# Kernel optimization log

Measured on AMD Instinct MI355X. Metric: run time of the kernel, lower is better.

Reference implementation:

```python
import jax, jax.numpy as jnp
import numpy as np

EPS = 1e-4
B, C, H, W = 8, 192, 64, 64
HID, DE, N_CLS, CLS_F, E = 256, 64, 8192, 128, 131072
N_IMG = B * H * W


def geolin(x, w):
    # MP_GeoLinear forward: weight-normalized linear, recomputed each call.
    fan = w.shape[1]
    n = jnp.linalg.norm(w, axis=1, keepdims=True)           # per-output-row norm (fp32)
    wn = w / (EPS + n / np.sqrt(fan))                       # normalize() with alpha=1/sqrt(fan)
    return x @ (wn * (1.0 / np.sqrt(fan))).T                # gain/sqrt(fan_in)


def mp_silu(x):
    return jax.nn.silu(x) / 0.596


def mp_cat(a, b, t=0.5):
    Na, Nb = a.shape[1], b.shape[1]
    Cc = np.sqrt((Na + Nb) / ((1 - t) ** 2 + t ** 2))
    return jnp.concatenate([(Cc / np.sqrt(Na) * (1 - t)) * a,
                            (Cc / np.sqrt(Nb) * t) * b], axis=1)


def hetero_conv(x_src, x_dst, src, dst, ea, wl, wr, n_dst):
    # MP_HIPGnnConv: gather -> mp_cat with edge_attr -> mean aggregate -> lin_l,
    # mp_sum with lin_r(x_dst) -> L2 normalize (normalize=True).
    msg = mp_cat(x_src[src], ea)                            # [E, HID+DE]
    s = jax.ops.segment_sum(msg, dst, num_segments=n_dst)
    cnt = jax.ops.segment_sum(jnp.ones((msg.shape[0],), msg.dtype), dst, num_segments=n_dst)
    agg = s / jnp.maximum(cnt, 1.0)[:, None]                # scatter-mean (empty rows -> 0)
    out = (geolin(agg, wl) + geolin(x_dst, wr)) / np.sqrt(2.0)  # mp_sum(t=0.5)
    return out / jnp.maximum(jnp.linalg.norm(out, axis=-1, keepdims=True), 1e-12)


def forward(x, class_x, ea_c2i, ea_i2c,
            w_in_img, w_in_cls,
            wl_c2i_1, wr_c2i_1, wl_i2c_1, wr_i2c_1,
            wl_c2i_2, wr_c2i_2, wl_i2c_2, wr_i2c_2,
            w_out_img, w_out_cls,
            src_c2i, dst_c2i, src_i2c, dst_i2c):
    b, c, h, w = x.shape
    n_img = b * h * w
    n_cls = class_x.shape[0]
    # image pixels become 'image_node' features: [B,C,H,W] -> [B*H*W, C]
    h_img = geolin(jnp.transpose(x, (0, 2, 3, 1)).reshape(-1, c), w_in_img)
    h_cls = geolin(class_x, w_in_cls)
    layers = [(wl_c2i_1, wr_c2i_1, wl_i2c_1, wr_i2c_1),
              (wl_c2i_2, wr_c2i_2, wl_i2c_2, wr_i2c_2)]
    for wl_ci, wr_ci, wl_ic, wr_ic in layers:
        a_img, a_cls = mp_silu(h_img), mp_silu(h_cls)
        h_img = hetero_conv(a_cls, a_img, src_c2i, dst_c2i, ea_c2i, wl_ci, wr_ci, n_img)
        h_cls = hetero_conv(a_img, a_cls, src_i2c, dst_i2c, ea_i2c, wl_ic, wr_ic, n_cls)
    out_img = geolin(h_img, w_out_img).reshape(b, h, w, -1)
    out_img = jnp.transpose(out_img, (0, 3, 1, 2))          # extract_image_nodes
    out_cls = geolin(h_cls, w_out_cls)
    return out_img, out_cls


def setup_inputs() -> dict:
    key = jax.random.key(0)
    ks = jax.random.split(key, 24)
    d = {
        'x': jax.random.normal(ks[0], (B, C, H, W), jnp.float32),
        'class_x': jax.random.normal(ks[1], (N_CLS, CLS_F), jnp.float32),
        'ea_c2i': jax.random.normal(ks[2], (E, DE), jnp.float32),
        'ea_i2c': jax.random.normal(ks[3], (E, DE), jnp.float32),
        'w_in_img': jax.random.normal(ks[4], (HID, C), jnp.float32),
        'w_in_cls': jax.random.normal(ks[5], (HID, CLS_F), jnp.float32),
        'wl_c2i_1': jax.random.normal(ks[6], (HID, HID + DE), jnp.float32),
        'wr_c2i_1': jax.random.normal(ks[7], (HID, HID), jnp.float32),
        'wl_i2c_1': jax.random.normal(ks[8], (HID, HID + DE), jnp.float32),
        'wr_i2c_1': jax.random.normal(ks[9], (HID, HID), jnp.float32),
        'wl_c2i_2': jax.random.normal(ks[10], (HID, HID + DE), jnp.float32),
        'wr_c2i_2': jax.random.normal(ks[11], (HID, HID), jnp.float32),
        'wl_i2c_2': jax.random.normal(ks[12], (HID, HID + DE), jnp.float32),
        'wr_i2c_2': jax.random.normal(ks[13], (HID, HID), jnp.float32),
        'w_out_img': jax.random.normal(ks[14], (HID, HID), jnp.float32),
        'w_out_cls': jax.random.normal(ks[15], (HID, HID), jnp.float32),
        'src_c2i': jax.random.randint(ks[16], (E,), 0, N_CLS, jnp.int32),
        'dst_c2i': jax.random.randint(ks[17], (E,), 0, N_IMG, jnp.int32),
        'src_i2c': jax.random.randint(ks[18], (E,), 0, N_IMG, jnp.int32),
        'dst_i2c': jax.random.randint(ks[19], (E,), 0, N_CLS, jnp.int32),
    }
    return d


def reference(x, class_x, ea_c2i, ea_i2c,
              w_in_img, w_in_cls,
              wl_c2i_1, wr_c2i_1, wl_i2c_1, wr_i2c_1,
              wl_c2i_2, wr_c2i_2, wl_i2c_2, wr_i2c_2,
              w_out_img, w_out_cls,
              src_c2i, dst_c2i, src_i2c, dst_i2c):
    return forward(x, class_x, ea_c2i, ea_i2c,
                   w_in_img, w_in_cls,
                   wl_c2i_1, wr_c2i_1, wl_i2c_1, wr_i2c_1,
                   wl_c2i_2, wr_c2i_2, wl_i2c_2, wr_i2c_2,
                   w_out_img, w_out_cls,
                   src_c2i, dst_c2i, src_i2c, dst_i2c)
```

## Files before the change

### kernel.cpp

```cpp
#include <hip/hip_runtime.h>
#include <cmath>

constexpr int CIN  = 192;
constexpr int HW   = 4096;
constexpr int NIMG = 32768;
constexpr int NCLS = 8192;
constexpr int NE   = 131072;

#define EPSW 1e-4f
#define ALPHA 0.7905694150420949f
#define BETA  1.5811388300841898f
#define SILU_INV 1.6778523489932886f

using bf16x8 = __attribute__((ext_vector_type(8))) __bf16;
using f32x4  = __attribute__((ext_vector_type(4))) float;

__device__ __forceinline__ ushort f2bf(float f) {
  uint u = __float_as_uint(f);
  u = (u + 0x7FFFu + ((u >> 16) & 1u)) >> 16;
  return (ushort)u;
}
__device__ __forceinline__ float bf2f(ushort h) {
  return __uint_as_float(((uint)h) << 16);
}
__device__ __forceinline__ float bflo(uint u) { return __uint_as_float(u << 16); }
__device__ __forceinline__ float bfhi(uint u) { return __uint_as_float(u & 0xFFFF0000u); }
__device__ __forceinline__ uint bfpack(float lo, float hi) {
  return (uint)f2bf(lo) | ((uint)f2bf(hi) << 16);
}
__device__ __forceinline__ float wave_red_sum(float v) {
  #pragma unroll
  for (int off = 32; off > 0; off >>= 1) v += __shfl_xor(v, off, 64);
  return v;
}
__device__ __forceinline__ int wave_red_sumi(int v) {
  #pragma unroll
  for (int off = 32; off > 0; off >>= 1) v += __shfl_xor(v, off, 64);
  return v;
}

struct WNA {
  const float* w[12];
  ushort* o[12];
  int F[12];
  int os[12];
  int oo[12];
};
__global__ __launch_bounds__(256) void pre_k(WNA a,
                                             const int* __restrict__ d1,
                                             const int* __restrict__ d2,
                                             int* __restrict__ c1,
                                             int* __restrict__ c2,
                                             const float* __restrict__ x,
                                             ushort* __restrict__ Xin,
                                             const float* __restrict__ clsx,
                                             ushort* __restrict__ clsb) {
  __shared__ ushort T[192 * 65];
  const int bx = blockIdx.x, t = threadIdx.x;
  if (bx < 768) {
    const int wi = bx >> 6;
    const int row = ((bx & 63) << 2) + (t >> 6);
    const int lane = t & 63;
    const int F = a.F[wi];
    const float* wr = a.w[wi] + (size_t)row * F;
    float ss = 0.f;
    for (int f = lane; f < F; f += 64) { float v = wr[f]; ss += v * v; }
    ss = wave_red_sum(ss);
    const float scale = 1.0f / (EPSW * sqrtf((float)F) + sqrtf(ss));
    ushort* o = a.o[wi] + (size_t)row * a.os[wi] + a.oo[wi];
    for (int f = lane; f < F; f += 64) o[f] = f2bf(wr[f] * scale);
  } else if (bx < 1280) {
    const int e = (bx - 768) * 256 + t;
    atomicAdd(&c1[d1[e]], 1);
    atomicAdd(&c2[d2[e]], 1);
  } else if (bx < 1792) {
    const int b2 = bx - 1280;
    const int b = b2 >> 6, hw0 = (b2 & 63) * 64;
    const float* xb = x + (size_t)b * CIN * HW;
    for (int idx = t; idx < CIN * 64; idx += 256) {
      int c = idx >> 6, p = idx & 63;
      T[c * 65 + p] = f2bf(xb[(size_t)c * HW + hw0 + p]);
    }
    __syncthreads();
    ushort* ob = Xin + ((size_t)b * HW + hw0) * CIN;
    for (int idx = t; idx < CIN * 64; idx += 256) {
      int p = idx / CIN, c = idx - p * CIN;
      ob[(size_t)p * CIN + c] = T[c * 65 + p];
    }
  } else {
    const int b3 = bx - 1792;
    for (int i4 = b3 * 256 + t; i4 < (NCLS * 128) / 4; i4 += 128 * 256) {
      float4 v = *(const float4*)(clsx + (size_t)i4 * 4);
      ushort4 o = { f2bf(v.x), f2bf(v.y), f2bf(v.z), f2bf(v.w) };
      *(ushort4*)(clsb + (size_t)i4 * 4) = o;
    }
  }
}

__global__ __launch_bounds__(256) void scanA_k(const int* __restrict__ cnt,
                                               int* __restrict__ st_img,
                                               int* __restrict__ st_cls,
                                               int* __restrict__ bsum) {
  const int bid = blockIdx.x;
  const bool cls = bid >= 32;
  const int* c = cnt + (cls ? NIMG : 0);
  int* s = cls ? st_cls : st_img;
  const int base = (cls ? bid - 32 : bid) * 1024;
  const int t = threadIdx.x, lane = t & 63, wid = t >> 6;
  int4 v = *(const int4*)(c + base + t * 4);
  const int i0 = v.x, i1 = i0 + v.y, i2 = i1 + v.z, i3 = i2 + v.w;
  int x = i3;
  #pragma unroll
  for (int off = 1; off < 64; off <<= 1) {
    int y = __shfl_up(x, off, 64);
    if (lane >= off) x += y;
  }
  const int pre = x - i3;
  __shared__ int wt[4];
  if (lane == 63) wt[wid] = x;
  __syncthreads();
  int woff = 0;
  #pragma unroll
  for (int i = 0; i < 4; ++i) if (i < wid) woff += wt[i];
  const int b = woff + pre;
  int4 o = { b, b + i0, b + i1, b + i2 };
  *(int4*)(s + base + t * 4) = o;
  if (t == 255) bsum[bid] = woff + x;
}

__global__ __launch_bounds__(256) void scanC_k(const int* __restrict__ bsum,
                                               int* __restrict__ st_img,
                                               int* __restrict__ st_cls) {
  const int bid = blockIdx.x;
  const bool cls = bid >= 32;
  const int seg0 = cls ? 32 : 0;
  const int t = threadIdx.x;
  __shared__ int off_s;
  if (t < 64) {
    int v = (t < bid - seg0) ? bsum[seg0 + t] : 0;
    v = wave_red_sumi(v);
    if (t == 0) off_s = v;
  }
  __syncthreads();
  const int off = off_s;
  int* s = cls ? st_cls : st_img;
  const int base = (cls ? bid - 32 : bid) * 1024;
  int4 v = *(int4*)(s + base + t * 4);
  v.x += off; v.y += off; v.z += off; v.w += off;
  *(int4*)(s + base + t * 4) = v;
  if (bid == 0 && t == 0) { st_img[NIMG] = NE; st_cls[NCLS] = NE; }
}

__global__ void fill2_k(const int* __restrict__ dst1, const int* __restrict__ src1,
                        const int* __restrict__ st1, int* __restrict__ cur1,
                        int2* __restrict__ eix1,
                        const int* __restrict__ dst2, const int* __restrict__ src2,
                        const int* __restrict__ st2, int* __restrict__ cur2,
                        int2* __restrict__ eix2) {
  int e = blockIdx.x * 256 + threadIdx.x;
  int d = dst1[e];
  int p = atomicAdd(&cur1[d], 1);
  eix1[st1[d] + p] = make_int2(e, src1[e]);
  d = dst2[e];
  p = atomicAdd(&cur2[d], 1);
  eix2[st2[d] + p] = make_int2(e, src2[e]);
}

__global__ void silu2_k(const ushort* __restrict__ Hi, const ushort* __restrict__ Hc,
                        ushort* __restrict__ Ai, ushort* __restrict__ Ac) {
  const size_t nimg = (size_t)NIMG * 256;
  size_t i8 = ((size_t)blockIdx.x * 256 + threadIdx.x) * 8;
  const ushort* in; ushort* out; size_t idx;
  if (i8 < nimg) { in = Hi; out = Ai; idx = i8; }
  else           { in = Hc; out = Ac; idx = i8 - nimg; }
  uint4 v = *(const uint4*)(in + idx);
  uint r[4];
  uint uu[4] = { v.x, v.y, v.z, v.w };
  #pragma unroll
  for (int i = 0; i < 4; ++i) {
    float lo = bflo(uu[i]), hi = bfhi(uu[i]);
    lo = (lo / (1.0f + __expf(-lo))) * SILU_INV;
    hi = (hi / (1.0f + __expf(-hi))) * SILU_INV;
    r[i] = bfpack(lo, hi);
  }
  uint4 o = { r[0], r[1], r[2], r[3] };
  *(uint4*)(out + idx) = o;
}

__global__ __launch_bounds__(256) void rownorm2_k(ushort* __restrict__ Hi,
                                                  ushort* __restrict__ Hc) {
  const int row  = blockIdx.x * 4 + (threadIdx.x >> 6);
  const int lane = threadIdx.x & 63;
  ushort* H = (row < NIMG) ? Hi + (size_t)row * 256
                           : Hc + (size_t)(row - NIMG) * 256;
  uint2 v = *(uint2*)(H + lane * 4);
  float x0 = bflo(v.x), x1 = bfhi(v.x), x2 = bflo(v.y), x3 = bfhi(v.y);
  float ss = x0 * x0 + x1 * x1 + x2 * x2 + x3 * x3;
  ss = wave_red_sum(ss);
  const float sc = 1.0f / fmaxf(sqrtf(ss), 1e-12f);
  uint2 o = { bfpack(x0 * sc, x1 * sc), bfpack(x2 * sc, x3 * sc) };
  *(uint2*)(H + lane * 4) = o;
}

__global__ __launch_bounds__(256) void agg2_k(
    const ushort* __restrict__ Aimg, const ushort* __restrict__ Acls,
    const int2* __restrict__ eix_ci, const int2* __restrict__ eix_ic,
    const int* __restrict__ st_img, const int* __restrict__ st_cls,
    ushort* __restrict__ agg_img, ushort* __restrict__ agg_cls,
    const float* __restrict__ ea_ci, const float* __restrict__ ea_ic,
    ushort* __restrict__ eam_img, ushort* __restrict__ eam_cls, int do_eam) {
  const int row = blockIdx.x * 8 + (threadIdx.x >> 5);
  const int hl  = threadIdx.x & 31;
  const ushort* Hs; const int2* eix; const int* st; ushort* out;
  const float* EA; ushort* oute; int r;
  if (row < NIMG) { r = row;        Hs = Acls; eix = eix_ci; st = st_img;
                    out = agg_img + (size_t)r * 256; EA = ea_ci;
                    oute = eam_img + (size_t)r * 64; }
  else            { r = row - NIMG; Hs = Aimg; eix = eix_ic; st = st_cls;
                    out = agg_cls + (size_t)r * 256; EA = ea_ic;
                    oute = eam_cls + (size_t)r * 64; }
  const int s0 = st[r], s1 = st[r + 1];
  float a[8] = {};
  float ae0 = 0.f, ae1 = 0.f;
  for (int j = s0; j < s1; j += 4) {
    const int i1 = min(j + 1, s1 - 1), i2 = min(j + 2, s1 - 1), i3 = min(j + 3, s1 - 1);
    const int2 e0 = eix[j], e1 = eix[i1], e2 = eix[i2], e3 = eix[i3];
    const float w1 = (j + 1 < s1) ? 1.f : 0.f;
    const float w2 = (j + 2 < s1) ? 1.f : 0.f;
    const float w3 = (j + 3 < s1) ? 1.f : 0.f;
    uint4 h0 = *(const uint4*)(Hs + (size_t)e0.y * 256 + hl * 8);
    uint4 h1 = *(const uint4*)(Hs + (size_t)e1.y * 256 + hl * 8);
    uint4 h2 = *(const uint4*)(Hs + (size_t)e2.y * 256 + hl * 8);
    uint4 h3 = *(const uint4*)(Hs + (size_t)e3.y * 256 + hl * 8);
    const uint u0[4] = { h0.x, h0.y, h0.z, h0.w };
    const uint u1[4] = { h1.x, h1.y, h1.z, h1.w };
    const uint u2[4] = { h2.x, h2.y, h2.z, h2.w };
    const uint u3[4] = { h3.x, h3.y, h3.z, h3.w };
    #pragma unroll
    for (int i = 0; i < 4; ++i) {
      a[2 * i + 0] += bflo(u0[i]) + w1 * bflo(u1[i]) + w2 * bflo(u2[i]) + w3 * bflo(u3[i]);
      a[2 * i + 1] += bfhi(u0[i]) + w1 * bfhi(u1[i]) + w2 * bfhi(u2[i]) + w3 * bfhi(u3[i]);
    }
    if (do_eam) {
      float2 v0 = *(const float2*)(EA + (size_t)e0.x * 64 + hl * 2);
      float2 v1 = *(const float2*)(EA + (size_t)e1.x * 64 + hl * 2);
      float2 v2 = *(const float2*)(EA + (size_t)e2.x * 64 + hl * 2);
      float2 v3 = *(const float2*)(EA + (size_t)e3.x * 64 + hl * 2);
      ae0 += v0.x + w1 * v1.x + w2 * v2.x + w3 * v3.x;
      ae1 += v0.y + w1 * v1.y + w2 * v2.y + w3 * v3.y;
    }
  }
  const float inv = 1.0f / fmaxf((float)(s1 - s0), 1.0f);
  const float c = ALPHA * inv;
  uint4 o;
  o.x = bfpack(a[0] * c, a[1] * c);
  o.y = bfpack(a[2] * c, a[3] * c);
  o.z = bfpack(a[4] * c, a[5] * c);
  o.w = bfpack(a[6] * c, a[7] * c);
  *(uint4*)(out + hl * 8) = o;
  if (do_eam) {
    const float cb = BETA * inv;
    *(uint*)(oute + hl * 2) = bfpack(ae0 * cb, ae1 * cb);
  }
}

__device__ __forceinline__ int lds_swz(int row, int kbyte) {
  return ((row << 6) + kbyte) ^ ((row & 7) << 4);
}

struct GJ {
  const ushort* A; const ushort* AG; const ushort* EAM; const ushort* B;
  void* O;
  int K, a_mode, c_mode, nrt;
};

__device__ __forceinline__ void gemm_body(const GJ J, int bx, char* ldsb) {
  ushort* As = (ushort*)ldsb;
  ushort* Bs = (ushort*)(ldsb + 8192);
  const int t    = threadIdx.x;
  const int row0 = (bx % J.nrt) * 128;
  const int col0 = (bx / J.nrt) * 128;
  const int srow = t >> 1;
  const int skh  = (t & 1) * 16;
  const int w    = t >> 6, lane = t & 63;
  const int wr   = (w >> 1) * 64, wc = (w & 1) * 64;
  const int l15  = lane & 15, lk16 = (lane >> 4) * 16;
  const int K = J.K;
  f32x4 acc[4][4] = {};

  uint4 ar0, ar1, br0, br1;
  auto loadA = [&](int k0) {
    const int row = row0 + srow;
    const int kk = k0 + skh;
    const ushort* p;
    if (J.a_mode == 2) {
      p = (kk < 256) ? J.AG + (size_t)row * 256 + kk
        : (kk < 320) ? J.EAM + (size_t)row * 64 + (kk - 256)
                     : J.A + (size_t)row * 256 + (kk - 320);
    } else {
      p = J.A + (size_t)row * K + kk;
    }
    ar0 = *(const uint4*)(p);
    ar1 = *(const uint4*)(p + 8);
  };
  auto loadB = [&](int k0) {
    const ushort* p = J.B + (size_t)(col0 + srow) * K + k0 + skh;
    br0 = *(const uint4*)(p);
    br1 = *(const uint4*)(p + 8);
  };

  loadA(0); loadB(0);
  for (int k0 = 0; k0 < K; k0 += 32) {
    __syncthreads();
    *(uint4*)((char*)As + lds_swz(srow, skh * 2))      = ar0;
    *(uint4*)((char*)As + lds_swz(srow, skh * 2 + 16)) = ar1;
    *(uint4*)((char*)Bs + lds_swz(srow, skh * 2))      = br0;
    *(uint4*)((char*)Bs + lds_swz(srow, skh * 2 + 16)) = br1;
    __syncthreads();
    if (k0 + 32 < K) { loadA(k0 + 32); loadB(k0 + 32); }
    bf16x8 af[4], bfr[4];
    #pragma unroll
    for (int m = 0; m < 4; ++m)
      af[m] = *(const bf16x8*)((const char*)As + lds_swz(wr + m * 16 + l15, lk16));
    #pragma unroll
    for (int n = 0; n < 4; ++n)
      bfr[n] = *(const bf16x8*)((const char*)Bs + lds_swz(wc + n * 16 + l15, lk16));
    #pragma unroll
    for (int m = 0; m < 4; ++m)
      #pragma unroll
      for (int n = 0; n < 4; ++n)
        acc[m][n] = __builtin_amdgcn_mfma_f32_16x16x32_bf16(af[m], bfr[n], acc[m][n], 0, 0, 0);
  }

  ushort* Ob = (ushort*)J.O;
  float*  Of = (float*)J.O;
  #pragma unroll
  for (int m = 0; m < 4; ++m) {
    const int rbase = row0 + wr + m * 16 + (lane >> 4) * 4;
    #pragma unroll
    for (int n = 0; n < 4; ++n) {
      const int col = col0 + wc + n * 16 + l15;
      #pragma unroll
      for (int j = 0; j < 4; ++j) {
        const int r = rbase + j;
        if (J.c_mode == 0)
          Ob[(size_t)r * 256 + col] = f2bf(acc[m][n][j]);
        else if (J.c_mode == 1)
          Of[((size_t)(col >> 12) * 256 + r) * 4096 + (col & 4095)] = acc[m][n][j];
        else
          Of[(size_t)r * 256 + col] = acc[m][n][j];
      }
    }
  }
}

__global__ __launch_bounds__(256) void gemm2_k(GJ j0, GJ j1, int n0) {
  __shared__ char ldsb[16384];
  const int bx = blockIdx.x;
  if (bx < n0) gemm_body(j0, bx, ldsb);
  else         gemm_body(j1, bx - n0, ldsb);
}

extern "C" void kernel_launch(void* const* d_in, const int* in_sizes, int n_in,
                              void* d_out, int out_size, void* d_ws, size_t ws_size,
                              hipStream_t stream) {
  const float* x        = (const float*)d_in[0];
  const float* class_x  = (const float*)d_in[1];
  const float* ea_c2i   = (const float*)d_in[2];
  const float* ea_i2c   = (const float*)d_in[3];
  const int* src_c2i = (const int*)d_in[16];
  const int* dst_c2i = (const int*)d_in[17];
  const int* src_i2c = (const int*)d_in[18];
  const int* dst_i2c = (const int*)d_in[19];

  float* ws = (float*)d_ws;
  size_t off = 0;
  auto alloc = [&](size_t n) { float* p = ws + off; off += (n + 15) & ~(size_t)15; return p; };

  ushort* A_img   = (ushort*)alloc((size_t)NIMG * 128);
  ushort* A_cls   = (ushort*)alloc((size_t)NCLS * 128);
  ushort* H_img   = (ushort*)alloc((size_t)NIMG * 128);
  ushort* H_cls   = (ushort*)alloc((size_t)NCLS * 128);
  ushort* agg_img = (ushort*)alloc((size_t)NIMG * 128);
  ushort* agg_cls = (ushort*)alloc((size_t)NCLS * 128);
  ushort* eam_img = (ushort*)alloc((size_t)NIMG * 32);
  ushort* eam_cls = (ushort*)alloc((size_t)NCLS * 32);
  int* cnt       = (int*)alloc(2 * (NIMG + NCLS));
  int* cur       = cnt + (NIMG + NCLS);
  int* bsum      = (int*)alloc(48);
  int* st_img    = (int*)alloc(NIMG + 1 + NCLS + 1 + 14);
  int* st_cls    = st_img + NIMG + 1;
  int2* eix_c2i  = (int2*)alloc((size_t)NE * 2);
  int2* eix_i2c  = (int2*)alloc((size_t)NE * 2);
  ushort* wn_in_img  = (ushort*)alloc(256 * 96);
  ushort* wn_in_cls  = (ushort*)alloc(256 * 64);
  ushort* wcat0      = (ushort*)alloc(256 * 288);
  ushort* wcat1      = (ushort*)alloc(256 * 288);
  ushort* wcat2      = (ushort*)alloc(256 * 288);
  ushort* wcat3      = (ushort*)alloc(256 * 288);
  ushort* wn_out_img = (ushort*)alloc(256 * 128);
  ushort* wn_out_cls = (ushort*)alloc(256 * 128);
  ushort* Xin      = agg_img;
  ushort* class_bf = agg_cls;

  const dim3 blk(256);

  hipMemsetAsync(cnt, 0, (size_t)2 * (NIMG + NCLS) * sizeof(int), stream);
  WNA wa;
  const float* wsrc[12] = { (const float*)d_in[4], (const float*)d_in[5],
                            (const float*)d_in[6], (const float*)d_in[7],
                            (const float*)d_in[8], (const float*)d_in[9],
                            (const float*)d_in[10], (const float*)d_in[11],
                            (const float*)d_in[12], (const float*)d_in[13],
                            (const float*)d_in[14], (const float*)d_in[15] };
  ushort* wdst[12] = { wn_in_img, wn_in_cls, wcat0, wcat0, wcat1, wcat1,
                       wcat2, wcat2, wcat3, wcat3, wn_out_img, wn_out_cls };
  const int wF[12]  = { 192, 128, 320, 256, 320, 256, 320, 256, 320, 256, 256, 256 };
  const int wOS[12] = { 192, 128, 576, 576, 576, 576, 576, 576, 576, 576, 256, 256 };
  const int wOO[12] = { 0, 0, 0, 320, 0, 320, 0, 320, 0, 320, 0, 0 };
  for (int i = 0; i < 12; ++i) {
    wa.w[i] = wsrc[i]; wa.o[i] = wdst[i]; wa.F[i] = wF[i]; wa.os[i] = wOS[i]; wa.oo[i] = wOO[i];
  }
  pre_k<<<1920, blk, 0, stream>>>(wa, dst_c2i, dst_i2c, cnt, cnt + NIMG,
                                  x, Xin, class_x, class_bf);

  scanA_k<<<40, blk, 0, stream>>>(cnt, st_img, st_cls, bsum);
  scanC_k<<<40, blk, 0, stream>>>(bsum, st_img, st_cls);
  fill2_k<<<NE / 256, blk, 0, stream>>>(dst_c2i, src_c2i, st_img, cur, eix_c2i,
                                        dst_i2c, src_i2c, st_cls, cur + NIMG, eix_i2c);

  GJ jin0 = { Xin,      nullptr, nullptr, wn_in_img, H_img, 192, 0, 0, 256 };
  GJ jin1 = { class_bf, nullptr, nullptr, wn_in_cls, H_cls, 128, 0, 0, 64 };
  gemm2_k<<<640, blk, 0, stream>>>(jin0, jin1, 512);

  const ushort* wc2i[2] = { wcat0, wcat2 };
  const ushort* wi2c[2] = { wcat1, wcat3 };
  for (int l = 0; l < 2; ++l) {
    silu2_k<<<((size_t)(NIMG + NCLS) * 256) / (8 * 256), blk, 0, stream>>>(
        H_img, H_cls, A_img, A_cls);
    agg2_k<<<(NIMG + NCLS) / 8, blk, 0, stream>>>(
        A_img, A_cls, eix_c2i, eix_i2c, st_img, st_cls, agg_img, agg_cls,
        ea_c2i, ea_i2c, eam_img, eam_cls, l == 0 ? 1 : 0);
    GJ jc0 = { A_img, agg_img, eam_img, wc2i[l], H_img, 576, 2, 0, 256 };
    GJ jc1 = { A_cls, agg_cls, eam_cls, wi2c[l], H_cls, 576, 2, 0, 64 };
    gemm2_k<<<640, blk, 0, stream>>>(jc0, jc1, 512);
    rownorm2_k<<<(NIMG + NCLS) / 4, blk, 0, stream>>>(H_img, H_cls);
  }

  float* out_img = (float*)d_out;
  float* out_cls = (float*)d_out + (size_t)NIMG * 256;
  GJ jo0 = { wn_out_img, nullptr, nullptr, H_img,      out_img, 256, 0, 1, 2 };
  GJ jo1 = { H_cls,      nullptr, nullptr, wn_out_cls, out_cls, 256, 0, 2, 64 };
  gemm2_k<<<640, blk, 0, stream>>>(jo0, jo1, 512);
}
```

Baseline: 222.9 us.

## Fuse SiLU into GEMM/rownorm epilogues and co-schedule independent stages

Removes the standalone SiLU pass. SiLU is now applied in the input GEMM epilogue, writing activations directly, and in the rownorm kernel, which writes both the normalized H and its SiLU. The per-layer schedule is reordered so that independent work shares one launch: the image GEMM runs alongside class aggregation, the class GEMM alongside image rownorm, and the output image GEMM alongside class rownorm. This saves a full read/write pass over activations and exposes cross-stage concurrency, at the cost of more launches with unequal block types and heterogeneous block workloads.

```diff
diff --git a/kernel.cpp b/kernel.cpp
--- a/kernel.cpp
+++ b/kernel.cpp
@@ -166,72 +166,28 @@
   eix2[st2[d] + p] = make_int2(e, src2[e]);
 }
 
-__global__ void silu2_k(const ushort* __restrict__ Hi, const ushort* __restrict__ Hc,
-                        ushort* __restrict__ Ai, ushort* __restrict__ Ac) {
-  const size_t nimg = (size_t)NIMG * 256;
-  size_t i8 = ((size_t)blockIdx.x * 256 + threadIdx.x) * 8;
-  const ushort* in; ushort* out; size_t idx;
-  if (i8 < nimg) { in = Hi; out = Ai; idx = i8; }
-  else           { in = Hc; out = Ac; idx = i8 - nimg; }
-  uint4 v = *(const uint4*)(in + idx);
-  uint r[4];
-  uint uu[4] = { v.x, v.y, v.z, v.w };
-  #pragma unroll
-  for (int i = 0; i < 4; ++i) {
-    float lo = bflo(uu[i]), hi = bfhi(uu[i]);
-    lo = (lo / (1.0f + __expf(-lo))) * SILU_INV;
-    hi = (hi / (1.0f + __expf(-hi))) * SILU_INV;
-    r[i] = bfpack(lo, hi);
-  }
-  uint4 o = { r[0], r[1], r[2], r[3] };
-  *(uint4*)(out + idx) = o;
-}
-
-__global__ __launch_bounds__(256) void rownorm2_k(ushort* __restrict__ Hi,
-                                                  ushort* __restrict__ Hc) {
-  const int row  = blockIdx.x * 4 + (threadIdx.x >> 6);
-  const int lane = threadIdx.x & 63;
-  ushort* H = (row < NIMG) ? Hi + (size_t)row * 256
-                           : Hc + (size_t)(row - NIMG) * 256;
-  uint2 v = *(uint2*)(H + lane * 4);
-  float x0 = bflo(v.x), x1 = bfhi(v.x), x2 = bflo(v.y), x3 = bfhi(v.y);
-  float ss = x0 * x0 + x1 * x1 + x2 * x2 + x3 * x3;
-  ss = wave_red_sum(ss);
-  const float sc = 1.0f / fmaxf(sqrtf(ss), 1e-12f);
-  uint2 o = { bfpack(x0 * sc, x1 * sc), bfpack(x2 * sc, x3 * sc) };
-  *(uint2*)(H + lane * 4) = o;
-}
-
-__global__ __launch_bounds__(256) void agg2_k(
-    const ushort* __restrict__ Aimg, const ushort* __restrict__ Acls,
-    const int2* __restrict__ eix_ci, const int2* __restrict__ eix_ic,
-    const int* __restrict__ st_img, const int* __restrict__ st_cls,
-    ushort* __restrict__ agg_img, ushort* __restrict__ agg_cls,
-    const float* __restrict__ ea_ci, const float* __restrict__ ea_ic,
-    ushort* __restrict__ eam_img, ushort* __restrict__ eam_cls, int do_eam) {
-  const int row = blockIdx.x * 8 + (threadIdx.x >> 5);
-  const int hl  = threadIdx.x & 31;
-  const ushort* Hs; const int2* eix; const int* st; ushort* out;
-  const float* EA; ushort* oute; int r;
-  if (row < NIMG) { r = row;        Hs = Acls; eix = eix_ci; st = st_img;
-                    out = agg_img + (size_t)r * 256; EA = ea_ci;
-                    oute = eam_img + (size_t)r * 64; }
-  else            { r = row - NIMG; Hs = Aimg; eix = eix_ic; st = st_cls;
-                    out = agg_cls + (size_t)r * 256; EA = ea_ic;
-                    oute = eam_cls + (size_t)r * 64; }
-  const int s0 = st[r], s1 = st[r + 1];
+struct AJ {
+  const ushort* Hs; const int2* eix; const int* st;
+  ushort* agg; const float* EA; ushort* eam; int do_eam;
+};
+
+__device__ __forceinline__ void agg_body(const AJ J, int bx, int t) {
+  const int r  = bx * 8 + (t >> 5);
+  const int hl = t & 31;
+  ushort* out = J.agg + (size_t)r * 256;
+  const int s0 = J.st[r], s1 = J.st[r + 1];
   float a[8] = {};
   float ae0 = 0.f, ae1 = 0.f;
   for (int j = s0; j < s1; j += 4) {
     const int i1 = min(j + 1, s1 - 1), i2 = min(j + 2, s1 - 1), i3 = min(j + 3, s1 - 1);
-    const int2 e0 = eix[j], e1 = eix[i1], e2 = eix[i2], e3 = eix[i3];
+    const int2 e0 = J.eix[j], e1 = J.eix[i1], e2 = J.eix[i2], e3 = J.eix[i3];
     const float w1 = (j + 1 < s1) ? 1.f : 0.f;
     const float w2 = (j + 2 < s1) ? 1.f : 0.f;
     const float w3 = (j + 3 < s1) ? 1.f : 0.f;
-    uint4 h0 = *(const uint4*)(Hs + (size_t)e0.y * 256 + hl * 8);
-    uint4 h1 = *(const uint4*)(Hs + (size_t)e1.y * 256 + hl * 8);
-    uint4 h2 = *(const uint4*)(Hs + (size_t)e2.y * 256 + hl * 8);
-    uint4 h3 = *(const uint4*)(Hs + (size_t)e3.y * 256 + hl * 8);
+    uint4 h0 = *(const uint4*)(J.Hs + (size_t)e0.y * 256 + hl * 8);
+    uint4 h1 = *(const uint4*)(J.Hs + (size_t)e1.y * 256 + hl * 8);
+    uint4 h2 = *(const uint4*)(J.Hs + (size_t)e2.y * 256 + hl * 8);
+    uint4 h3 = *(const uint4*)(J.Hs + (size_t)e3.y * 256 + hl * 8);
     const uint u0[4] = { h0.x, h0.y, h0.z, h0.w };
     const uint u1[4] = { h1.x, h1.y, h1.z, h1.w };
     const uint u2[4] = { h2.x, h2.y, h2.z, h2.w };
@@ -241,11 +197,11 @@
       a[2 * i + 0] += bflo(u0[i]) + w1 * bflo(u1[i]) + w2 * bflo(u2[i]) + w3 * bflo(u3[i]);
       a[2 * i + 1] += bfhi(u0[i]) + w1 * bfhi(u1[i]) + w2 * bfhi(u2[i]) + w3 * bfhi(u3[i]);
     }
-    if (do_eam) {
-      float2 v0 = *(const float2*)(EA + (size_t)e0.x * 64 + hl * 2);
-      float2 v1 = *(const float2*)(EA + (size_t)e1.x * 64 + hl * 2);
-      float2 v2 = *(const float2*)(EA + (size_t)e2.x * 64 + hl * 2);
-      float2 v3 = *(const float2*)(EA + (size_t)e3.x * 64 + hl * 2);
+    if (J.do_eam) {
+      float2 v0 = *(const float2*)(J.EA + (size_t)e0.x * 64 + hl * 2);
+      float2 v1 = *(const float2*)(J.EA + (size_t)e1.x * 64 + hl * 2);
+      float2 v2 = *(const float2*)(J.EA + (size_t)e2.x * 64 + hl * 2);
+      float2 v3 = *(const float2*)(J.EA + (size_t)e3.x * 64 + hl * 2);
       ae0 += v0.x + w1 * v1.x + w2 * v2.x + w3 * v3.x;
       ae1 += v0.y + w1 * v1.y + w2 * v2.y + w3 * v3.y;
     }
@@ -258,9 +214,33 @@
   o.z = bfpack(a[4] * c, a[5] * c);
   o.w = bfpack(a[6] * c, a[7] * c);
   *(uint4*)(out + hl * 8) = o;
-  if (do_eam) {
+  if (J.do_eam) {
     const float cb = BETA * inv;
-    *(uint*)(oute + hl * 2) = bfpack(ae0 * cb, ae1 * cb);
+    *(uint*)(J.eam + (size_t)r * 64 + hl * 2) = bfpack(ae0 * cb, ae1 * cb);
+  }
+}
+
+struct RJ { ushort* H; ushort* A; int do_silu; };
+
+__device__ __forceinline__ void rns_body(const RJ J, int bx, int t) {
+  const int row  = bx * 4 + (t >> 6);
+  const int lane = t & 63;
+  ushort* H = J.H + (size_t)row * 256;
+  uint2 v = *(uint2*)(H + lane * 4);
+  float x0 = bflo(v.x), x1 = bfhi(v.x), x2 = bflo(v.y), x3 = bfhi(v.y);
+  float ss = x0 * x0 + x1 * x1 + x2 * x2 + x3 * x3;
+  ss = wave_red_sum(ss);
+  const float sc = 1.0f / fmaxf(sqrtf(ss), 1e-12f);
+  x0 *= sc; x1 *= sc; x2 *= sc; x3 *= sc;
+  uint2 o = { bfpack(x0, x1), bfpack(x2, x3) };
+  *(uint2*)(H + lane * 4) = o;
+  if (J.do_silu) {
+    float s0 = (x0 / (1.0f + __expf(-x0))) * SILU_INV;
+    float s1 = (x1 / (1.0f + __expf(-x1))) * SILU_INV;
+    float s2 = (x2 / (1.0f + __expf(-x2))) * SILU_INV;
+    float s3 = (x3 / (1.0f + __expf(-x3))) * SILU_INV;
+    uint2 oa = { bfpack(s0, s1), bfpack(s2, s3) };
+    *(uint2*)(J.A + (size_t)row * 256 + lane * 4) = oa;
   }
 }
 
@@ -271,7 +251,7 @@
 struct GJ {
   const ushort* A; const ushort* AG; const ushort* EAM; const ushort* B;
   void* O;
-  int K, a_mode, c_mode, nrt;
+  int K, a_mode, c_mode, nrt, do_silu;
 };
 
 __device__ __forceinline__ void gemm_body(const GJ J, int bx, char* ldsb) {
@@ -343,12 +323,15 @@
       #pragma unroll
       for (int j = 0; j < 4; ++j) {
         const int r = rbase + j;
-        if (J.c_mode == 0)
-          Ob[(size_t)r * 256 + col] = f2bf(acc[m][n][j]);
-        else if (J.c_mode == 1)
+        if (J.c_mode == 0) {
+          float v = acc[m][n][j];
+          if (J.do_silu) v = (v / (1.0f + __expf(-v))) * SILU_INV;
+          Ob[(size_t)r * 256 + col] = f2bf(v);
+        } else if (J.c_mode == 1) {
           Of[((size_t)(col >> 12) * 256 + r) * 4096 + (col & 4095)] = acc[m][n][j];
-        else
+        } else {
           Of[(size_t)r * 256 + col] = acc[m][n][j];
+        }
       }
     }
   }
@@ -359,6 +342,28 @@
   const int bx = blockIdx.x;
   if (bx < n0) gemm_body(j0, bx, ldsb);
   else         gemm_body(j1, bx - n0, ldsb);
+}
+
+__global__ __launch_bounds__(256) void gemm_agg_k(GJ g, AJ a, int ng) {
+  __shared__ char ldsb[16384];
+  const int bx = blockIdx.x;
+  if (bx < ng) gemm_body(g, bx, ldsb);
+  else         agg_body(a, bx - ng, threadIdx.x);
+}
+
+__global__ __launch_bounds__(256) void gemm_rns_k(GJ g, RJ r, int ng) {
+  __shared__ char ldsb[16384];
+  const int bx = blockIdx.x;
+  if (bx < ng) gemm_body(g, bx, ldsb);
+  else         rns_body(r, bx - ng, threadIdx.x);
+}
+
+__global__ __launch_bounds__(256) void agg_k(AJ a) {
+  agg_body(a, blockIdx.x, threadIdx.x);
+}
+
+__global__ __launch_bounds__(256) void rns_k(RJ r) {
+  rns_body(r, blockIdx.x, threadIdx.x);
 }
 
 extern "C" void kernel_launch(void* const* d_in, const int* in_sizes, int n_in,
@@ -429,27 +434,44 @@
   fill2_k<<<NE / 256, blk, 0, stream>>>(dst_c2i, src_c2i, st_img, cur, eix_c2i,
                                         dst_i2c, src_i2c, st_cls, cur + NIMG, eix_i2c);
 
-  GJ jin0 = { Xin,      nullptr, nullptr, wn_in_img, H_img, 192, 0, 0, 256 };
-  GJ jin1 = { class_bf, nullptr, nullptr, wn_in_cls, H_cls, 128, 0, 0, 64 };
+  GJ jin0 = { Xin,      nullptr, nullptr, wn_in_img, A_img, 192, 0, 0, 256, 1 };
+  GJ jin1 = { class_bf, nullptr, nullptr, wn_in_cls, A_cls, 128, 0, 0, 64, 1 };
   gemm2_k<<<640, blk, 0, stream>>>(jin0, jin1, 512);
 
   const ushort* wc2i[2] = { wcat0, wcat2 };
   const ushort* wi2c[2] = { wcat1, wcat3 };
-  for (int l = 0; l < 2; ++l) {
-    silu2_k<<<((size_t)(NIMG + NCLS) * 256) / (8 * 256), blk, 0, stream>>>(
-        H_img, H_cls, A_img, A_cls);
-    agg2_k<<<(NIMG + NCLS) / 8, blk, 0, stream>>>(
-        A_img, A_cls, eix_c2i, eix_i2c, st_img, st_cls, agg_img, agg_cls,
-        ea_c2i, ea_i2c, eam_img, eam_cls, l == 0 ? 1 : 0);
-    GJ jc0 = { A_img, agg_img, eam_img, wc2i[l], H_img, 576, 2, 0, 256 };
-    GJ jc1 = { A_cls, agg_cls, eam_cls, wi2c[l], H_cls, 576, 2, 0, 64 };
-    gemm2_k<<<640, blk, 0, stream>>>(jc0, jc1, 512);
-    rownorm2_k<<<(NIMG + NCLS) / 4, blk, 0, stream>>>(H_img, H_cls);
-  }
+
+  AJ aI0 = { A_cls, eix_c2i, st_img, agg_img, ea_c2i, eam_img, 1 };
+  agg_k<<<NIMG / 8, blk, 0, stream>>>(aI0);
+
+  GJ gI0 = { A_img, agg_img, eam_img, wc2i[0], H_img, 576, 2, 0, 256, 0 };
+  AJ aC0 = { A_img, eix_i2c, st_cls, agg_cls, ea_i2c, eam_cls, 1 };
+  gemm_agg_k<<<512 + NCLS / 8, blk, 0, stream>>>(gI0, aC0, 512);
+
+  GJ gC0 = { A_cls, agg_cls, eam_cls, wi2c[0], H_cls, 576, 2, 0, 64, 0 };
+  RJ rIs = { H_img, A_img, 1 };
+  gemm_rns_k<<<128 + NIMG / 4, blk, 0, stream>>>(gC0, rIs, 128);
+
+  RJ rCs = { H_cls, A_cls, 1 };
+  rns_k<<<NCLS / 4, blk, 0, stream>>>(rCs);
+
+  AJ aI1 = { A_cls, eix_c2i, st_img, agg_img, nullptr, nullptr, 0 };
+  agg_k<<<NIMG / 8, blk, 0, stream>>>(aI1);
+
+  GJ gI1 = { A_img, agg_img, eam_img, wc2i[1], H_img, 576, 2, 0, 256, 0 };
+  AJ aC1 = { A_img, eix_i2c, st_cls, agg_cls, nullptr, nullptr, 0 };
+  gemm_agg_k<<<512 + NCLS / 8, blk, 0, stream>>>(gI1, aC1, 512);
+
+  GJ gC1 = { A_cls, agg_cls, eam_cls, wi2c[1], H_cls, 576, 2, 0, 64, 0 };
+  RJ rI1 = { H_img, nullptr, 0 };
+  gemm_rns_k<<<128 + NIMG / 4, blk, 0, stream>>>(gC1, rI1, 128);
 
   float* out_img = (float*)d_out;
   float* out_cls = (float*)d_out + (size_t)NIMG * 256;
-  GJ jo0 = { wn_out_img, nullptr, nullptr, H_img,      out_img, 256, 0, 1, 2 };
-  GJ jo1 = { H_cls,      nullptr, nullptr, wn_out_cls, out_cls, 256, 0, 2, 64 };
-  gemm2_k<<<640, blk, 0, stream>>>(jo0, jo1, 512);
-}
+  GJ joI = { wn_out_img, nullptr, nullptr, H_img, out_img, 256, 0, 1, 2, 0 };
+  RJ rC1 = { H_cls, nullptr, 0 };
+  gemm_rns_k<<<512 + NCLS / 4, blk, 0, stream>>>(joI, rC1, 512);
+
+  GJ joC = { H_cls, nullptr, nullptr, wn_out_cls, out_cls, 256, 0, 2, 64, 0 };
+  gemm2_k<<<128, blk, 0, stream>>>(joC, joC, 128);
+}
```

Result: slower. 237.5 us (+6.6%).

## Fuse SiLU into GEMM epilogue and rownorm, merge edge fill into input GEMM

Applied to the files above, without the earlier changes.

Removes the standalone SiLU kernels. The input projection GEMM now writes SiLU activations directly, and the layer-1 row-normalize kernel also emits the SiLU'd copy for layer 2. The CSR edge-fill work is folded into the input GEMM launch as extra blocks, so the two independent jobs run together. This drops two full elementwise passes over the node features and a couple of launches, at the cost of extra exp work in the GEMM epilogue and a more branchy kernel.

```diff
diff --git a/kernel.cpp b/kernel.cpp
--- a/kernel.cpp
+++ b/kernel.cpp
@@ -151,55 +151,17 @@
   if (bid == 0 && t == 0) { st_img[NIMG] = NE; st_cls[NCLS] = NE; }
 }
 
-__global__ void fill2_k(const int* __restrict__ dst1, const int* __restrict__ src1,
-                        const int* __restrict__ st1, int* __restrict__ cur1,
-                        int2* __restrict__ eix1,
-                        const int* __restrict__ dst2, const int* __restrict__ src2,
-                        const int* __restrict__ st2, int* __restrict__ cur2,
-                        int2* __restrict__ eix2) {
-  int e = blockIdx.x * 256 + threadIdx.x;
+__device__ __forceinline__ void fill_body(
+    int e, const int* __restrict__ dst1, const int* __restrict__ src1,
+    const int* __restrict__ st1, int* __restrict__ cur1, int2* __restrict__ eix1,
+    const int* __restrict__ dst2, const int* __restrict__ src2,
+    const int* __restrict__ st2, int* __restrict__ cur2, int2* __restrict__ eix2) {
   int d = dst1[e];
   int p = atomicAdd(&cur1[d], 1);
   eix1[st1[d] + p] = make_int2(e, src1[e]);
   d = dst2[e];
   p = atomicAdd(&cur2[d], 1);
   eix2[st2[d] + p] = make_int2(e, src2[e]);
-}
-
-__global__ void silu2_k(const ushort* __restrict__ Hi, const ushort* __restrict__ Hc,
-                        ushort* __restrict__ Ai, ushort* __restrict__ Ac) {
-  const size_t nimg = (size_t)NIMG * 256;
-  size_t i8 = ((size_t)blockIdx.x * 256 + threadIdx.x) * 8;
-  const ushort* in; ushort* out; size_t idx;
-  if (i8 < nimg) { in = Hi; out = Ai; idx = i8; }
-  else           { in = Hc; out = Ac; idx = i8 - nimg; }
-  uint4 v = *(const uint4*)(in + idx);
-  uint r[4];
-  uint uu[4] = { v.x, v.y, v.z, v.w };
-  #pragma unroll
-  for (int i = 0; i < 4; ++i) {
-    float lo = bflo(uu[i]), hi = bfhi(uu[i]);
-    lo = (lo / (1.0f + __expf(-lo))) * SILU_INV;
-    hi = (hi / (1.0f + __expf(-hi))) * SILU_INV;
-    r[i] = bfpack(lo, hi);
-  }
-  uint4 o = { r[0], r[1], r[2], r[3] };
-  *(uint4*)(out + idx) = o;
-}
-
-__global__ __launch_bounds__(256) void rownorm2_k(ushort* __restrict__ Hi,
-                                                  ushort* __restrict__ Hc) {
-  const int row  = blockIdx.x * 4 + (threadIdx.x >> 6);
-  const int lane = threadIdx.x & 63;
-  ushort* H = (row < NIMG) ? Hi + (size_t)row * 256
-                           : Hc + (size_t)(row - NIMG) * 256;
-  uint2 v = *(uint2*)(H + lane * 4);
-  float x0 = bflo(v.x), x1 = bfhi(v.x), x2 = bflo(v.y), x3 = bfhi(v.y);
-  float ss = x0 * x0 + x1 * x1 + x2 * x2 + x3 * x3;
-  ss = wave_red_sum(ss);
-  const float sc = 1.0f / fmaxf(sqrtf(ss), 1e-12f);
-  uint2 o = { bfpack(x0 * sc, x1 * sc), bfpack(x2 * sc, x3 * sc) };
-  *(uint2*)(H + lane * 4) = o;
 }
 
 __global__ __launch_bounds__(256) void agg2_k(
@@ -264,6 +226,34 @@
   }
 }
 
+__global__ __launch_bounds__(256) void rns2_k(ushort* __restrict__ Hi,
+                                              ushort* __restrict__ Hc,
+                                              ushort* __restrict__ Ai,
+                                              ushort* __restrict__ Ac,
+                                              int do_silu) {
+  const int row  = blockIdx.x * 4 + (threadIdx.x >> 6);
+  const int lane = threadIdx.x & 63;
+  ushort* H; ushort* A;
+  if (row < NIMG) { H = Hi + (size_t)row * 256; A = Ai + (size_t)row * 256; }
+  else { H = Hc + (size_t)(row - NIMG) * 256; A = Ac + (size_t)(row - NIMG) * 256; }
+  uint2 v = *(uint2*)(H + lane * 4);
+  float x0 = bflo(v.x), x1 = bfhi(v.x), x2 = bflo(v.y), x3 = bfhi(v.y);
+  float ss = x0 * x0 + x1 * x1 + x2 * x2 + x3 * x3;
+  ss = wave_red_sum(ss);
+  const float sc = 1.0f / fmaxf(sqrtf(ss), 1e-12f);
+  x0 *= sc; x1 *= sc; x2 *= sc; x3 *= sc;
+  uint2 o = { bfpack(x0, x1), bfpack(x2, x3) };
+  *(uint2*)(H + lane * 4) = o;
+  if (do_silu) {
+    float s0 = (x0 / (1.0f + __expf(-x0))) * SILU_INV;
+    float s1 = (x1 / (1.0f + __expf(-x1))) * SILU_INV;
+    float s2 = (x2 / (1.0f + __expf(-x2))) * SILU_INV;
+    float s3 = (x3 / (1.0f + __expf(-x3))) * SILU_INV;
+    uint2 oa = { bfpack(s0, s1), bfpack(s2, s3) };
+    *(uint2*)(A + lane * 4) = oa;
+  }
+}
+
 __device__ __forceinline__ int lds_swz(int row, int kbyte) {
   return ((row << 6) + kbyte) ^ ((row & 7) << 4);
 }
@@ -271,7 +261,7 @@
 struct GJ {
   const ushort* A; const ushort* AG; const ushort* EAM; const ushort* B;
   void* O;
-  int K, a_mode, c_mode, nrt;
+  int K, a_mode, c_mode, nrt, do_silu;
 };
 
 __device__ __forceinline__ void gemm_body(const GJ J, int bx, char* ldsb) {
@@ -343,12 +333,15 @@
       #pragma unroll
       for (int j = 0; j < 4; ++j) {
         const int r = rbase + j;
-        if (J.c_mode == 0)
-          Ob[(size_t)r * 256 + col] = f2bf(acc[m][n][j]);
-        else if (J.c_mode == 1)
+        if (J.c_mode == 0) {
+          float v = acc[m][n][j];
+          if (J.do_silu) v = (v / (1.0f + __expf(-v))) * SILU_INV;
+          Ob[(size_t)r * 256 + col] = f2bf(v);
+        } else if (J.c_mode == 1) {
           Of[((size_t)(col >> 12) * 256 + r) * 4096 + (col & 4095)] = acc[m][n][j];
-        else
+        } else {
           Of[(size_t)r * 256 + col] = acc[m][n][j];
+        }
       }
     }
   }
@@ -359,6 +352,20 @@
   const int bx = blockIdx.x;
   if (bx < n0) gemm_body(j0, bx, ldsb);
   else         gemm_body(j1, bx - n0, ldsb);
+}
+
+__global__ __launch_bounds__(256) void gemm_fill_k(
+    GJ j0, GJ j1,
+    const int* dst1, const int* src1, const int* st1, int* cur1, int2* eix1,
+    const int* dst2, const int* src2, const int* st2, int* cur2, int2* eix2) {
+  __shared__ char ldsb[16384];
+  const int bx = blockIdx.x;
+  if (bx < 512)      gemm_body(j0, bx, ldsb);
+  else if (bx < 640) gemm_body(j1, bx - 512, ldsb);
+  else {
+    const int e = (bx - 640) * 256 + threadIdx.x;
+    fill_body(e, dst1, src1, st1, cur1, eix1, dst2, src2, st2, cur2, eix2);
+  }
 }
 
 extern "C" void kernel_launch(void* const* d_in, const int* in_sizes, int n_in,
@@ -426,30 +433,29 @@
 
   scanA_k<<<40, blk, 0, stream>>>(cnt, st_img, st_cls, bsum);
   scanC_k<<<40, blk, 0, stream>>>(bsum, st_img, st_cls);
-  fill2_k<<<NE / 256, blk, 0, stream>>>(dst_c2i, src_c2i, st_img, cur, eix_c2i,
+
+  GJ jin0 = { Xin,      nullptr, nullptr, wn_in_img, A_img, 192, 0, 0, 256, 1 };
+  GJ jin1 = { class_bf, nullptr, nullptr, wn_in_cls, A_cls, 128, 0, 0, 64, 1 };
+  gemm_fill_k<<<1152, blk, 0, stream>>>(jin0, jin1,
+                                        dst_c2i, src_c2i, st_img, cur, eix_c2i,
                                         dst_i2c, src_i2c, st_cls, cur + NIMG, eix_i2c);
-
-  GJ jin0 = { Xin,      nullptr, nullptr, wn_in_img, H_img, 192, 0, 0, 256 };
-  GJ jin1 = { class_bf, nullptr, nullptr, wn_in_cls, H_cls, 128, 0, 0, 64 };
-  gemm2_k<<<640, blk, 0, stream>>>(jin0, jin1, 512);
 
   const ushort* wc2i[2] = { wcat0, wcat2 };
   const ushort* wi2c[2] = { wcat1, wcat3 };
   for (int l = 0; l < 2; ++l) {
-    silu2_k<<<((size_t)(NIMG + NCLS) * 256) / (8 * 256), blk, 0, stream>>>(
-        H_img, H_cls, A_img, A_cls);
     agg2_k<<<(NIMG + NCLS) / 8, blk, 0, stream>>>(
         A_img, A_cls, eix_c2i, eix_i2c, st_img, st_cls, agg_img, agg_cls,
         ea_c2i, ea_i2c, eam_img, eam_cls, l == 0 ? 1 : 0);
-    GJ jc0 = { A_img, agg_img, eam_img, wc2i[l], H_img, 576, 2, 0, 256 };
-    GJ jc1 = { A_cls, agg_cls, eam_cls, wi2c[l], H_cls, 576, 2, 0, 64 };
+    GJ jc0 = { A_img, agg_img, eam_img, wc2i[l], H_img, 576, 2, 0, 256, 0 };
+    GJ jc1 = { A_cls, agg_cls, eam_cls, wi2c[l], H_cls, 576, 2, 0, 64, 0 };
     gemm2_k<<<640, blk, 0, stream>>>(jc0, jc1, 512);
-    rownorm2_k<<<(NIMG + NCLS) / 4, blk, 0, stream>>>(H_img, H_cls);
+    rns2_k<<<(NIMG + NCLS) / 4, blk, 0, stream>>>(H_img, H_cls, A_img, A_cls,
+                                                  l == 0 ? 1 : 0);
   }
 
   float* out_img = (float*)d_out;
   float* out_cls = (float*)d_out + (size_t)NIMG * 256;
-  GJ jo0 = { wn_out_img, nullptr, nullptr, H_img,      out_img, 256, 0, 1, 2 };
-  GJ jo1 = { H_cls,      nullptr, nullptr, wn_out_cls, out_cls, 256, 0, 2, 64 };
+  GJ jo0 = { wn_out_img, nullptr, nullptr, H_img,      out_img, 256, 0, 1, 2, 0 };
+  GJ jo1 = { H_cls,      nullptr, nullptr, wn_out_cls, out_cls, 256, 0, 2, 64, 0 };
   gemm2_k<<<640, blk, 0, stream>>>(jo0, jo1, 512);
 }
```

Result: faster. 209.7 us (-5.9%).
